# Kernel optimization log

Hardware: AMD Instinct MI355X
Metric: run time of the kernel (lower is better)

The kernel has to match this reference:

```python
import jax, jax.numpy as jnp
import numpy as np
import math

B, S, E, H, FF = 2, 2048, 1024, 16, 4096
HD = E // H
EPS = 1e-6


def layer_norm(x, gamma, beta):
    mu = jnp.mean(x, axis=-1, keepdims=True)
    var = jnp.mean(jnp.square(x - mu), axis=-1, keepdims=True)
    return (x - mu) * jax.lax.rsqrt(var + EPS) * gamma + beta


def setup_inputs() -> dict:
    key = jax.random.key(0)
    ks = jax.random.split(key, 8)
    x_embeds = jax.random.normal(ks[0], (B, S, E), dtype=jnp.float32)
    # causal mask: True means masked (j > i), broadcastable over batch/heads
    mask = jnp.triu(jnp.ones((S, S), dtype=bool), k=1)[None, None]
    sc = 1.0 / math.sqrt(E)
    w_kqv = jax.random.normal(ks[1], (3 * E, E), dtype=jnp.float32) * sc
    w_o = jax.random.normal(ks[2], (E, E), dtype=jnp.float32) * sc
    w_up = jax.random.normal(ks[3], (FF, E), dtype=jnp.float32) * sc
    b_up = jnp.zeros((FF,), dtype=jnp.float32)
    w_down = jax.random.normal(ks[4], (E, FF), dtype=jnp.float32) / math.sqrt(FF)
    b_down = jnp.zeros((E,), dtype=jnp.float32)
    g1 = jnp.ones((E,), dtype=jnp.float32)
    b1 = jnp.zeros((E,), dtype=jnp.float32)
    g2 = jnp.ones((E,), dtype=jnp.float32)
    b2 = jnp.zeros((E,), dtype=jnp.float32)
    return {"x_embeds": x_embeds, "mask": mask, "w_kqv": w_kqv, "w_o": w_o,
            "w_up": w_up, "b_up": b_up, "w_down": w_down, "b_down": b_down,
            "g1": g1, "b1": b1, "g2": g2, "b2": b2}


def reference(x_embeds, mask, w_kqv, w_o, w_up, b_up, w_down, b_down, g1, b1, g2, b2):
    b, s = x_embeds.shape[0], x_embeds.shape[1]
    # --- attention ---
    kqv = x_embeds @ w_kqv.T                      # [B,S,3E]
    kqv = kqv.reshape(b, s, 3, H, HD).transpose(0, 3, 2, 1, 4)  # [B,H,3,S,HD]
    xk, xq, xv = kqv[:, :, 0], kqv[:, :, 1], kqv[:, :, 2]
    attn = jnp.einsum('bhqd,bhkd->bhqk', xq, xk) / math.sqrt(HD)
    attn = jnp.where(mask, -jnp.inf, attn)
    attn = jax.nn.softmax(attn, axis=-1)
    out = jnp.einsum('bhqk,bhkd->bhqd', attn, xv)  # [B,H,S,HD]
    out = out.transpose(0, 2, 1, 3).reshape(b, s, E)
    out = out @ w_o.T
    x = layer_norm(out + x_embeds, g1, b1)
    # --- ffnn ---
    h = jax.nn.relu(x @ w_up.T + b_up)
    h = h @ w_down.T + b_down
    return layer_norm(h + x, g2, b2)
```

## Files before the change

kernel.cpp:

```cpp
#include <hip/hip_runtime.h>
#include <stdint.h>

#define B_ 2
#define S_ 2048
#define E_ 1024
#define H_ 16
#define HD_ 64
#define FF_ 4096
#define M_ 4096
#define LOG2E_ 1.44269504f

typedef short bf16x8 __attribute__((ext_vector_type(8)));
typedef float f32x4  __attribute__((ext_vector_type(4)));
typedef short shortx4 __attribute__((ext_vector_type(4)));

#define MFMA16(a,b,c) __builtin_amdgcn_mfma_f32_16x16x32_bf16(a,b,c,0,0,0)

__device__ __forceinline__ short f2bf(float f) {
  uint32_t u = __builtin_bit_cast(uint32_t, f);
  u += 0x7fffu + ((u >> 16) & 1u);
  return (short)(u >> 16);
}
__device__ __forceinline__ float bf2f(short b) {
  uint32_t u = ((uint32_t)(uint16_t)b) << 16;
  return __builtin_bit_cast(float, u);
}
__device__ __forceinline__ float exp2_hw(float x) {
  float r;
  asm("v_exp_f32 %0, %1" : "=v"(r) : "v"(x));
  return r;
}

template<int CTRL>
__device__ __forceinline__ float dpp_ror(float x) {
  return __builtin_bit_cast(float,
    __builtin_amdgcn_update_dpp(0, __builtin_bit_cast(int, x), CTRL, 0xF, 0xF, true));
}
__device__ __forceinline__ float dpp_max16(float v) {
  v = fmaxf(v, dpp_ror<0x128>(v));
  v = fmaxf(v, dpp_ror<0x124>(v));
  v = fmaxf(v, dpp_ror<0x122>(v));
  v = fmaxf(v, dpp_ror<0x121>(v));
  return v;
}
__device__ __forceinline__ float dpp_sum16(float v) {
  v += dpp_ror<0x128>(v);
  v += dpp_ror<0x124>(v);
  v += dpp_ror<0x122>(v);
  v += dpp_ror<0x121>(v);
  return v;
}

#define GLDS16(g, l) __builtin_amdgcn_global_load_lds( \
    (const __attribute__((address_space(1))) unsigned int*)(g), \
    (__attribute__((address_space(3))) unsigned int*)(l), 16, 0, 0)

__global__ void cast_all(const float* __restrict__ x, const float* __restrict__ wkqv,
                         const float* __restrict__ wo, const float* __restrict__ wup,
                         const float* __restrict__ wdown,
                         short* __restrict__ xb, short* __restrict__ wkqvb,
                         short* __restrict__ wob, short* __restrict__ wupb,
                         short* __restrict__ wdownb) {
  const int stride = gridDim.x * blockDim.x;
  for (int i = blockIdx.x * blockDim.x + threadIdx.x; i < 4194304; i += stride) {
    const int e = i << 2;
    const float* src; short* dst; int off;
    if (e < 4194304)       { src = x;     dst = xb;     off = e; }
    else if (e < 7340032)  { src = wkqv;  dst = wkqvb;  off = e - 4194304; }
    else if (e < 8388608)  { src = wo;    dst = wob;    off = e - 7340032; }
    else if (e < 12582912) { src = wup;   dst = wupb;   off = e - 8388608; }
    else                   { src = wdown; dst = wdownb; off = e - 12582912; }
    float4 v = *(const float4*)(src + off);
    shortx4 o;
    o.x = f2bf(v.x); o.y = f2bf(v.y); o.z = f2bf(v.z); o.w = f2bf(v.w);
    *(shortx4*)(dst + off) = o;
  }
}

template<int SK, int EPI, typename OutT>
__global__ __launch_bounds__(256) void gemm_bt(
    const short* __restrict__ A, const short* __restrict__ Bw,
    OutT* __restrict__ C0, OutT* __restrict__ C1, const float* __restrict__ bias,
    int M, int N, int K)
{
  __shared__ short Al[2][128 * 32];
  __shared__ short Bl[2][128 * 32];
  const int tid  = threadIdx.x;
  const int w    = tid >> 6, lane = tid & 63;
  const int ntiles = N >> 7;
  const int nwg = gridDim.x;
  const int bid = blockIdx.x;
  const int swz = (bid & 7) * (nwg >> 3) + (bid >> 3);
  const int tn = swz % ntiles, tm = swz / ntiles;
  const int m0 = tm << 7, n0 = tn << 7;
  const int wr = (w >> 1) << 6, wc = (w & 1) << 6;
  const int lr = lane & 15, lk = (lane >> 4) << 3;
  const int ra = lane >> 2, colA = (lane & 3) << 3;

  const int kper = K / SK;
  const int kbeg = (SK > 1) ? (int)blockIdx.y * kper : 0;
  const int T = kper >> 5;
  OutT* __restrict__ C = (SK > 1 && blockIdx.y) ? C1 : C0;

  const short* Ag0 = A  + (size_t)(m0 + w * 16 + ra) * K + colA;
  const short* Ag1 = A  + (size_t)(m0 + (w + 4) * 16 + ra) * K + colA;
  const short* Bg0 = Bw + (size_t)(n0 + w * 16 + ra) * K + colA;
  const short* Bg1 = Bw + (size_t)(n0 + (w + 4) * 16 + ra) * K + colA;

  f32x4 acc[4][4] = {};

  {
    const int k0 = kbeg;
    GLDS16(Ag0 + k0, &Al[0][w * 512]);
    GLDS16(Ag1 + k0, &Al[0][(w + 4) * 512]);
    GLDS16(Bg0 + k0, &Bl[0][w * 512]);
    GLDS16(Bg1 + k0, &Bl[0][(w + 4) * 512]);
  }

  for (int it = 0; it < T; ++it) {
    const int buf = it & 1;
    if (it + 1 < T) {
      const int k1 = kbeg + ((it + 1) << 5);
      GLDS16(Ag0 + k1, &Al[buf ^ 1][w * 512]);
      GLDS16(Ag1 + k1, &Al[buf ^ 1][(w + 4) * 512]);
      GLDS16(Bg0 + k1, &Bl[buf ^ 1][w * 512]);
      GLDS16(Bg1 + k1, &Bl[buf ^ 1][(w + 4) * 512]);
      asm volatile("s_waitcnt vmcnt(4)" ::: "memory");
    } else {
      asm volatile("s_waitcnt vmcnt(0)" ::: "memory");
    }
    __builtin_amdgcn_sched_barrier(0);
    __builtin_amdgcn_s_barrier();

    bf16x8 af[4], bfr[4];
    #pragma unroll
    for (int i = 0; i < 4; ++i)
      af[i] = *(const bf16x8*)&Al[buf][(wr + i * 16 + lr) * 32 + lk];
    #pragma unroll
    for (int j = 0; j < 4; ++j)
      bfr[j] = *(const bf16x8*)&Bl[buf][(wc + j * 16 + lr) * 32 + lk];
    #pragma unroll
    for (int i = 0; i < 4; ++i)
      #pragma unroll
      for (int j = 0; j < 4; ++j)
        acc[i][j] = MFMA16(af[i], bfr[j], acc[i][j]);

    __builtin_amdgcn_s_barrier();
  }

  const int lg = lane >> 4;
  #pragma unroll
  for (int j = 0; j < 4; ++j) {
    const int col = n0 + wc + j * 16 + lr;
    float bv = 0.f;
    if constexpr (SK == 1 && EPI != 0) bv = bias[col];
    #pragma unroll
    for (int i = 0; i < 4; ++i) {
      #pragma unroll
      for (int r = 0; r < 4; ++r) {
        const int row = m0 + wr + i * 16 + lg * 4 + r;
        float v = acc[i][j][r] + bv;
        if constexpr (SK == 1 && EPI == 1) v = fmaxf(v, 0.f);
        if constexpr (sizeof(OutT) == 2) C[(size_t)row * N + col] = f2bf(v);
        else                             C[(size_t)row * N + col] = v;
      }
    }
  }
}

__global__ __launch_bounds__(512) void attn_kernel(
    const short* __restrict__ kqv, short* __restrict__ out)
{
  __shared__ short Kt[2][64][72];
  __shared__ short Vt[2][64][72];
  __shared__ short Pl[8][16][72];

  const int tid = threadIdx.x, w = tid >> 6, lane = tid & 63;
  const int wt = w & 3;
  const int p = blockIdx.x;
  const int bh = blockIdx.y;
  const int b = bh >> 4, h = bh & 15;
  const int q0 = ((w < 4) ? (31 - p) : p) << 6;
  const int nkb = 32 - p;
  const int lr = lane & 15, lg = lane >> 4;

  const size_t rowq = (size_t)(b * S_ + q0 + wt * 16 + lr) * 3072 + 1024 + h * 64;
  bf16x8 qf[2];
  qf[0] = *(const bf16x8*)&kqv[rowq + lg * 8];
  qf[1] = *(const bf16x8*)&kqv[rowq + 32 + lg * 8];
  #pragma unroll
  for (int ks = 0; ks < 2; ++ks)
    #pragma unroll
    for (int e = 0; e < 8; ++e)
      qf[ks][e] = f2bf(bf2f(qf[ks][e]) * 0.125f);

  f32x4 acc[4] = {};
  float m_run[4], l_run[4];
  #pragma unroll
  for (int r = 0; r < 4; ++r) { m_run[r] = -1e30f; l_run[r] = 0.f; }

  const int skk = tid >> 3;
  const int sc  = (tid & 7) << 3;
  const int vws = (tid & 7) << 3;
  const int vkc = skk ^ vws;
  const short* gstage = kqv + (size_t)b * S_ * 3072 + h * 64 + sc;

  {
    bf16x8 kreg = *(const bf16x8*)&gstage[(size_t)skk * 3072];
    bf16x8 vreg = *(const bf16x8*)&gstage[(size_t)skk * 3072 + 2048];
    *(bf16x8*)&Kt[0][skk][sc] = kreg;
    #pragma unroll
    for (int e = 0; e < 8; ++e) Vt[0][sc + e][vkc] = vreg[e];
  }
  __syncthreads();

  for (int kbi = 0; kbi < nkb; ++kbi) {
    const int buf = kbi & 1;
    const int kb = kbi << 6;

    bf16x8 kreg, vreg;
    const bool more = (kbi + 1 < nkb);
    if (more) {
      const size_t gb = (size_t)(((kbi + 1) << 6) + skk) * 3072;
      kreg = *(const bf16x8*)&gstage[gb];
      vreg = *(const bf16x8*)&gstage[gb + 2048];
    }

    if (kb <= q0 + wt * 16 + 15) {
      f32x4 sacc[4] = {};
      __builtin_amdgcn_s_setprio(1);
      #pragma unroll
      for (int jt = 0; jt < 4; ++jt) {
        #pragma unroll
        for (int ks = 0; ks < 2; ++ks) {
          bf16x8 kf = *(const bf16x8*)&Kt[buf][jt * 16 + lr][ks * 32 + lg * 8];
          sacc[jt] = MFMA16(qf[ks], kf, sacc[jt]);
        }
      }
      __builtin_amdgcn_s_setprio(0);
      const bool full = (kb + 63 <= q0 + wt * 16);
      float rmax[4];
      if (full) {
        #pragma unroll
        for (int r = 0; r < 4; ++r)
          rmax[r] = fmaxf(fmaxf(sacc[0][r], sacc[1][r]), fmaxf(sacc[2][r], sacc[3][r]));
      } else {
        #pragma unroll
        for (int r = 0; r < 4; ++r) rmax[r] = -1e30f;
        #pragma unroll
        for (int jt = 0; jt < 4; ++jt) {
          const int kpos = kb + jt * 16 + lr;
          #pragma unroll
          for (int r = 0; r < 4; ++r) {
            const int qrow = q0 + wt * 16 + lg * 4 + r;
            float v = (kpos <= qrow) ? sacc[jt][r] : -1e30f;
            sacc[jt][r] = v;
            rmax[r] = fmaxf(rmax[r], v);
          }
        }
      }
      #pragma unroll
      for (int r = 0; r < 4; ++r) rmax[r] = dpp_max16(rmax[r]);
      int need = 0;
      #pragma unroll
      for (int r = 0; r < 4; ++r) need |= (rmax[r] > m_run[r] + 8.f) ? 1 : 0;
      if (__any(need)) {
        #pragma unroll
        for (int r = 0; r < 4; ++r) {
          const float mn = fmaxf(m_run[r], rmax[r]);
          const float al = exp2_hw((m_run[r] - mn) * LOG2E_);
          m_run[r] = mn;
          l_run[r] *= al;
          #pragma unroll
          for (int dt = 0; dt < 4; ++dt) acc[dt][r] *= al;
        }
      }
      float m2[4], rsum[4];
      #pragma unroll
      for (int r = 0; r < 4; ++r) { m2[r] = m_run[r] * LOG2E_; rsum[r] = 0.f; }
      #pragma unroll
      for (int jt = 0; jt < 4; ++jt)
        #pragma unroll
        for (int r = 0; r < 4; ++r) {
          const float pv = exp2_hw(__builtin_fmaf(sacc[jt][r], LOG2E_, -m2[r]));
          sacc[jt][r] = pv;
          rsum[r] += pv;
        }
      #pragma unroll
      for (int r = 0; r < 4; ++r) { rsum[r] = dpp_sum16(rsum[r]); l_run[r] += rsum[r]; }
      #pragma unroll
      for (int jt = 0; jt < 4; ++jt) {
        uint32_t w01, w23;
        asm("v_cvt_pk_bf16_f32 %0, %1, %2" : "=v"(w01) : "v"(sacc[jt][0]), "v"(sacc[jt][1]));
        asm("v_cvt_pk_bf16_f32 %0, %1, %2" : "=v"(w23) : "v"(sacc[jt][2]), "v"(sacc[jt][3]));
        Pl[w][lg * 4 + 0][jt * 16 + lr] = (short)(w01 & 0xffffu);
        Pl[w][lg * 4 + 1][jt * 16 + lr] = (short)(w01 >> 16);
        Pl[w][lg * 4 + 2][jt * 16 + lr] = (short)(w23 & 0xffffu);
        Pl[w][lg * 4 + 3][jt * 16 + lr] = (short)(w23 >> 16);
      }
      bf16x8 pa[2];
      pa[0] = *(const bf16x8*)&Pl[w][lr][lg * 8];
      pa[1] = *(const bf16x8*)&Pl[w][lr][32 + lg * 8];
      __builtin_amdgcn_s_setprio(1);
      #pragma unroll
      for (int dt = 0; dt < 4; ++dt) {
        const int vswz = (2 * dt + (lr >> 3)) << 3;
        #pragma unroll
        for (int ks = 0; ks < 2; ++ks) {
          bf16x8 vb = *(const bf16x8*)&Vt[buf][dt * 16 + lr][(ks * 32 + lg * 8) ^ vswz];
          acc[dt] = MFMA16(pa[ks], vb, acc[dt]);
        }
      }
      __builtin_amdgcn_s_setprio(0);
    }

    if (more) {
      *(bf16x8*)&Kt[buf ^ 1][skk][sc] = kreg;
      #pragma unroll
      for (int e = 0; e < 8; ++e) Vt[buf ^ 1][sc + e][vkc] = vreg[e];
    }
    __syncthreads();
  }

  #pragma unroll
  for (int dt = 0; dt < 4; ++dt) {
    #pragma unroll
    for (int r = 0; r < 4; ++r) {
      const int d = h * 64 + dt * 16 + lr;
      const int q_row = q0 + wt * 16 + lg * 4 + r;
      out[(size_t)(b * S_ + q_row) * E_ + d] = f2bf(acc[dt][r] / l_run[r]);
    }
  }
}

template<int FINAL>
__global__ __launch_bounds__(256) void ln_kernel(
    const float* __restrict__ y0, const float* __restrict__ y1,
    const float* __restrict__ bias, const void* __restrict__ res,
    const float* __restrict__ gam, const float* __restrict__ bet,
    void* __restrict__ outp)
{
  const int row = blockIdx.x, tid = threadIdx.x, lane = tid & 63, w = tid >> 6;
  float4 a = ((const float4*)(y0 + (size_t)row * E_))[tid];
  float4 c = ((const float4*)(y1 + (size_t)row * E_))[tid];
  float r[4] = {a.x + c.x, a.y + c.y, a.z + c.z, a.w + c.w};
  if constexpr (FINAL) {
    float4 bi = ((const float4*)bias)[tid];
    shortx4 rb = ((const shortx4*)((const short*)res + (size_t)row * E_))[tid];
    r[0] += bi.x + bf2f(rb.x); r[1] += bi.y + bf2f(rb.y);
    r[2] += bi.z + bf2f(rb.z); r[3] += bi.w + bf2f(rb.w);
  } else {
    float4 rv = ((const float4*)((const float*)res + (size_t)row * E_))[tid];
    r[0] += rv.x; r[1] += rv.y; r[2] += rv.z; r[3] += rv.w;
  }
  float s  = r[0] + r[1] + r[2] + r[3];
  float ss = r[0]*r[0] + r[1]*r[1] + r[2]*r[2] + r[3]*r[3];
  #pragma unroll
  for (int m = 32; m >= 1; m >>= 1) { s += __shfl_xor(s, m); ss += __shfl_xor(ss, m); }
  __shared__ float red[8];
  if (lane == 0) { red[w] = s; red[4 + w] = ss; }
  __syncthreads();
  s  = red[0] + red[1] + red[2] + red[3];
  ss = red[4] + red[5] + red[6] + red[7];
  const float mu  = s * (1.f / E_);
  const float var = ss * (1.f / E_) - mu * mu;
  const float rs  = rsqrtf(var + 1e-6f);
  float4 gv = ((const float4*)gam)[tid];
  float4 bv = ((const float4*)bet)[tid];
  float o0 = (r[0] - mu) * rs * gv.x + bv.x;
  float o1 = (r[1] - mu) * rs * gv.y + bv.y;
  float o2 = (r[2] - mu) * rs * gv.z + bv.z;
  float o3 = (r[3] - mu) * rs * gv.w + bv.w;
  if constexpr (FINAL) {
    float4 o; o.x = o0; o.y = o1; o.z = o2; o.w = o3;
    ((float4*)((float*)outp + (size_t)row * E_))[tid] = o;
  } else {
    shortx4 o; o.x = f2bf(o0); o.y = f2bf(o1); o.z = f2bf(o2); o.w = f2bf(o3);
    ((shortx4*)((short*)outp + (size_t)row * E_))[tid] = o;
  }
}

extern "C" void kernel_launch(void* const* d_in, const int* in_sizes, int n_in,
                              void* d_out, int out_size, void* d_ws, size_t ws_size,
                              hipStream_t stream) {
  const float* x      = (const float*)d_in[0];
  const float* w_kqv  = (const float*)d_in[2];
  const float* w_o    = (const float*)d_in[3];
  const float* w_up   = (const float*)d_in[4];
  const float* b_up   = (const float*)d_in[5];
  const float* w_down = (const float*)d_in[6];
  const float* b_down = (const float*)d_in[7];
  const float* g1     = (const float*)d_in[8];
  const float* b1     = (const float*)d_in[9];
  const float* g2     = (const float*)d_in[10];
  const float* b2     = (const float*)d_in[11];
  float* out = (float*)d_out;

  char* ws = (char*)d_ws;
  short* xb     = (short*)(ws);
  short* wkqvb  = (short*)(ws + ((size_t)8  << 20));
  short* wob    = (short*)(ws + ((size_t)14 << 20));
  short* wupb   = (short*)(ws + ((size_t)16 << 20));
  short* wdownb = (short*)(ws + ((size_t)24 << 20));
  short* kqv    = (short*)(ws + ((size_t)32 << 20));
  float* proj0  = (float*)(ws + ((size_t)32 << 20));
  float* proj1  = (float*)(ws + ((size_t)48 << 20));
  short* hbuf   = (short*)(ws + ((size_t)32 << 20));
  short* attno  = (short*)(ws + ((size_t)64 << 20));
  short* xln    = (short*)(ws + ((size_t)72 << 20));
  float* down0  = (float*)(ws);
  float* down1  = (float*)(ws + ((size_t)80 << 20));

  cast_all<<<2048, 256, 0, stream>>>(x, w_kqv, w_o, w_up, w_down,
                                     xb, wkqvb, wob, wupb, wdownb);

  gemm_bt<1, 0, short><<<24 * 32, 256, 0, stream>>>(xb, wkqvb, kqv, nullptr, nullptr, M_, 3 * E_, E_);
  attn_kernel<<<dim3(16, B_ * H_), 512, 0, stream>>>(kqv, attno);
  gemm_bt<2, 0, float><<<dim3(256, 2), 256, 0, stream>>>(attno, wob, proj0, proj1, nullptr, M_, E_, E_);
  ln_kernel<0><<<M_, 256, 0, stream>>>(proj0, proj1, nullptr, x, g1, b1, xln);
  gemm_bt<1, 1, short><<<32 * 32, 256, 0, stream>>>(xln, wupb, hbuf, nullptr, b_up, M_, FF_, E_);
  gemm_bt<2, 0, float><<<dim3(256, 2), 256, 0, stream>>>(hbuf, wdownb, down0, down1, nullptr, M_, E_, FF_);
  ln_kernel<1><<<M_, 256, 0, stream>>>(down0, down1, b_down, xln, g2, b2, out);
}
```

Baseline: 243.0 us.

## Add 256x256-tile 512-thread GEMM for QKV and up-projection

Adds a new bf16 GEMM kernel with 256x256 output tiles, 8 waves of 512 threads, K-step 64, a double-buffered LDS with swizzled layout, and global-to-LDS loads spread across four MFMA phases. The QKV and FFN-up GEMMs now use it instead of the 128x128 kernel. The goal is more data reuse per LDS load and better overlap of memory traffic with MFMA work. The cost is larger LDS use (128KB), many accumulator registers, and fewer workgroups (192 and 256), which may leave some of the 256 CUs idle for the QKV GEMM.

```diff
diff --git a/kernel.cpp b/kernel.cpp
--- a/kernel.cpp
+++ b/kernel.cpp
@@ -74,6 +74,169 @@
     shortx4 o;
     o.x = f2bf(v.x); o.y = f2bf(v.y); o.z = f2bf(v.z); o.w = f2bf(v.w);
     *(shortx4*)(dst + off) = o;
+  }
+}
+
+template<int EPI>
+__global__ __launch_bounds__(512, 2) void gemm256_bt(
+    const short* __restrict__ A, const short* __restrict__ Bw,
+    short* __restrict__ C, const float* __restrict__ bias,
+    int M, int N, int K)
+{
+  __shared__ short Al[2][16384];
+  __shared__ short Bl[2][16384];
+  const int tid = threadIdx.x;
+  const int w = tid >> 6, lane = tid & 63;
+  const int lr = lane & 15, lg = lane >> 4;
+  const int ntiles = N >> 8;
+  const int nwg = gridDim.x;
+  const int bid = blockIdx.x;
+  const int swz = (bid & 7) * (nwg >> 3) + (bid >> 3);
+  const int tn = swz % ntiles, tm = swz / ntiles;
+  const int m0 = tm << 8, n0 = tn << 8;
+  const int wrm = (w >> 2) << 7;
+  const int wcn = (w & 3) << 6;
+
+  const int srow = lane >> 3;
+  const int scol = ((lane & 7) ^ srow) << 3;
+  const short* Ag[4]; const short* Bg[4];
+  #pragma unroll
+  for (int i = 0; i < 4; ++i) {
+    const int c = w + i * 8;
+    Ag[i] = A  + (size_t)(m0 + c * 8 + srow) * K + scol;
+    Bg[i] = Bw + (size_t)(n0 + c * 8 + srow) * K + scol;
+  }
+
+  f32x4 acc[8][4] = {};
+  const int T = K >> 6;
+
+  #pragma unroll
+  for (int i = 0; i < 4; ++i) {
+    GLDS16(Ag[i], &Al[0][(w + i * 8) * 512]);
+    GLDS16(Bg[i], &Bl[0][(w + i * 8) * 512]);
+  }
+
+  for (int t = 0; t < T; ++t) {
+    const int buf = t & 1;
+    const bool more = (t + 1 < T);
+    const int k1 = (t + 1) << 6;
+
+    bf16x8 af[8], bf01[4], bf23[4];
+    const int ph0 = lg ^ (lr & 7);
+    const int ph1 = (4 + lg) ^ (lr & 7);
+
+    if (more) {
+      GLDS16(Ag[0] + k1, &Al[buf ^ 1][(w + 0) * 512]);
+      GLDS16(Ag[1] + k1, &Al[buf ^ 1][(w + 8) * 512]);
+      asm volatile("s_waitcnt vmcnt(2)" ::: "memory");
+    } else {
+      asm volatile("s_waitcnt vmcnt(0)" ::: "memory");
+    }
+    __builtin_amdgcn_sched_barrier(0);
+    __builtin_amdgcn_s_barrier();
+
+    #pragma unroll
+    for (int i = 0; i < 4; ++i) {
+      const int R = wrm + i * 16 + lr;
+      af[i * 2]     = *(const bf16x8*)&Al[buf][R * 64 + ph0 * 8];
+      af[i * 2 + 1] = *(const bf16x8*)&Al[buf][R * 64 + ph1 * 8];
+    }
+    #pragma unroll
+    for (int j = 0; j < 2; ++j) {
+      const int R = wcn + j * 16 + lr;
+      bf01[j * 2]     = *(const bf16x8*)&Bl[buf][R * 64 + ph0 * 8];
+      bf01[j * 2 + 1] = *(const bf16x8*)&Bl[buf][R * 64 + ph1 * 8];
+    }
+    __builtin_amdgcn_s_setprio(1);
+    #pragma unroll
+    for (int i = 0; i < 4; ++i)
+      #pragma unroll
+      for (int j = 0; j < 2; ++j) {
+        acc[i][j] = MFMA16(af[i * 2],     bf01[j * 2],     acc[i][j]);
+        acc[i][j] = MFMA16(af[i * 2 + 1], bf01[j * 2 + 1], acc[i][j]);
+      }
+    __builtin_amdgcn_s_setprio(0);
+    __builtin_amdgcn_s_barrier();
+
+    if (more) {
+      GLDS16(Ag[2] + k1, &Al[buf ^ 1][(w + 16) * 512]);
+      GLDS16(Ag[3] + k1, &Al[buf ^ 1][(w + 24) * 512]);
+    }
+    #pragma unroll
+    for (int j = 0; j < 2; ++j) {
+      const int R = wcn + (j + 2) * 16 + lr;
+      bf23[j * 2]     = *(const bf16x8*)&Bl[buf][R * 64 + ph0 * 8];
+      bf23[j * 2 + 1] = *(const bf16x8*)&Bl[buf][R * 64 + ph1 * 8];
+    }
+    __builtin_amdgcn_s_setprio(1);
+    #pragma unroll
+    for (int i = 0; i < 4; ++i)
+      #pragma unroll
+      for (int j = 0; j < 2; ++j) {
+        acc[i][j + 2] = MFMA16(af[i * 2],     bf23[j * 2],     acc[i][j + 2]);
+        acc[i][j + 2] = MFMA16(af[i * 2 + 1], bf23[j * 2 + 1], acc[i][j + 2]);
+      }
+    __builtin_amdgcn_s_setprio(0);
+    __builtin_amdgcn_s_barrier();
+
+    if (more) {
+      GLDS16(Bg[0] + k1, &Bl[buf ^ 1][(w + 0) * 512]);
+      GLDS16(Bg[1] + k1, &Bl[buf ^ 1][(w + 8) * 512]);
+    }
+    #pragma unroll
+    for (int i = 0; i < 4; ++i) {
+      const int R = wrm + (i + 4) * 16 + lr;
+      af[i * 2]     = *(const bf16x8*)&Al[buf][R * 64 + ph0 * 8];
+      af[i * 2 + 1] = *(const bf16x8*)&Al[buf][R * 64 + ph1 * 8];
+    }
+    __builtin_amdgcn_s_setprio(1);
+    #pragma unroll
+    for (int i = 0; i < 4; ++i)
+      #pragma unroll
+      for (int j = 0; j < 2; ++j) {
+        acc[i + 4][j + 2] = MFMA16(af[i * 2],     bf23[j * 2],     acc[i + 4][j + 2]);
+        acc[i + 4][j + 2] = MFMA16(af[i * 2 + 1], bf23[j * 2 + 1], acc[i + 4][j + 2]);
+      }
+    __builtin_amdgcn_s_setprio(0);
+    __builtin_amdgcn_s_barrier();
+
+    if (more) {
+      GLDS16(Bg[2] + k1, &Bl[buf ^ 1][(w + 16) * 512]);
+      GLDS16(Bg[3] + k1, &Bl[buf ^ 1][(w + 24) * 512]);
+    }
+    #pragma unroll
+    for (int j = 0; j < 2; ++j) {
+      const int R = wcn + j * 16 + lr;
+      bf01[j * 2]     = *(const bf16x8*)&Bl[buf][R * 64 + ph0 * 8];
+      bf01[j * 2 + 1] = *(const bf16x8*)&Bl[buf][R * 64 + ph1 * 8];
+    }
+    __builtin_amdgcn_s_setprio(1);
+    #pragma unroll
+    for (int i = 0; i < 4; ++i)
+      #pragma unroll
+      for (int j = 0; j < 2; ++j) {
+        acc[i + 4][j] = MFMA16(af[i * 2],     bf01[j * 2],     acc[i + 4][j]);
+        acc[i + 4][j] = MFMA16(af[i * 2 + 1], bf01[j * 2 + 1], acc[i + 4][j]);
+      }
+    __builtin_amdgcn_s_setprio(0);
+    __builtin_amdgcn_s_barrier();
+  }
+
+  #pragma unroll
+  for (int j = 0; j < 4; ++j) {
+    const int col = n0 + wcn + j * 16 + lr;
+    float bv = 0.f;
+    if constexpr (EPI == 1) bv = bias[col];
+    #pragma unroll
+    for (int i = 0; i < 8; ++i) {
+      #pragma unroll
+      for (int r = 0; r < 4; ++r) {
+        const int row = m0 + wrm + i * 16 + lg * 4 + r;
+        float v = acc[i][j][r] + bv;
+        if constexpr (EPI == 1) v = fmaxf(v, 0.f);
+        C[(size_t)row * N + col] = f2bf(v);
+      }
+    }
   }
 }
 
@@ -414,11 +577,11 @@
   cast_all<<<2048, 256, 0, stream>>>(x, w_kqv, w_o, w_up, w_down,
                                      xb, wkqvb, wob, wupb, wdownb);
 
-  gemm_bt<1, 0, short><<<24 * 32, 256, 0, stream>>>(xb, wkqvb, kqv, nullptr, nullptr, M_, 3 * E_, E_);
+  gemm256_bt<0><<<192, 512, 0, stream>>>(xb, wkqvb, kqv, nullptr, M_, 3 * E_, E_);
   attn_kernel<<<dim3(16, B_ * H_), 512, 0, stream>>>(kqv, attno);
   gemm_bt<2, 0, float><<<dim3(256, 2), 256, 0, stream>>>(attno, wob, proj0, proj1, nullptr, M_, E_, E_);
   ln_kernel<0><<<M_, 256, 0, stream>>>(proj0, proj1, nullptr, x, g1, b1, xln);
-  gemm_bt<1, 1, short><<<32 * 32, 256, 0, stream>>>(xln, wupb, hbuf, nullptr, b_up, M_, FF_, E_);
+  gemm256_bt<1><<<256, 512, 0, stream>>>(xln, wupb, hbuf, b_up, M_, FF_, E_);
   gemm_bt<2, 0, float><<<dim3(256, 2), 256, 0, stream>>>(hbuf, wdownb, down0, down1, nullptr, M_, E_, FF_);
   ln_kernel<1><<<M_, 256, 0, stream>>>(down0, down1, b_down, xln, g2, b2, out);
 }
```

Measured after the change: 256.5 us. 1.06x slower.
